# Kernel tuning notes

Hardware: AMD Instinct MI355X
Metric: run time of the kernel (lower is better)

Reference implementation:

```python
import jax, jax.numpy as jnp
import numpy as np

B, N = 32, 2048
SLOTS, PSD, VIEW = 5, 15, 9
DM, NH, MH, EGO = 64, 4, 128, 32
PAIR_D = SLOTS * (SLOTS - 1) // 2          # 10
TER_D = VIEW * VIEW                        # 81
NBR_D = SLOTS * PSD + PAIR_D               # 85
D_OBS = EGO + NBR_D + TER_D                # 198


def setup_inputs() -> dict:
    key = jax.random.key(0)
    ks = jax.random.split(key, 64)

    def _p(k, shape, s=0.05):
        return (jax.random.normal(k, shape) * s).astype(jnp.float32)

    def z(*shape):
        return jnp.zeros(shape, jnp.float32)

    # --- observation with some genuinely-masked slots (r == 0) ---
    ego = jax.random.normal(ks[0], (B, N, EGO), jnp.float32)
    nbr = jax.random.normal(ks[1], (B, N, SLOTS, PSD), jnp.float32)
    keep = jax.random.bernoulli(ks[2], 0.8, (B, N, SLOTS)).astype(jnp.float32)
    nbr = jnp.concatenate([nbr[..., 0:3] * keep[..., None], nbr[..., 3:]], axis=-1)
    pair = jax.random.normal(ks[3], (B, N, PAIR_D), jnp.float32)
    ter = jax.random.normal(ks[4], (B, N, TER_D), jnp.float32)
    obs = jnp.concatenate([ego, nbr.reshape(B, N, SLOTS * PSD), pair, ter], axis=-1)

    i = 5
    def nk():
        nonlocal i
        i += 1
        return ks[i - 1]

    params = {
        "tok_w": _p(nk(), (12, DM)), "tok_b": z(DM),
        "ln1_s": jnp.ones((DM,), jnp.float32), "ln1_b": z(DM),
        "a1_qw": _p(nk(), (DM, DM)), "a1_qb": z(DM),
        "a1_kw": _p(nk(), (DM, DM)), "a1_kb": z(DM),
        "a1_vw": _p(nk(), (DM, DM)), "a1_vb": z(DM),
        "a1_ow": _p(nk(), (DM, DM)), "a1_ob": z(DM),
        "ln2_s": jnp.ones((DM,), jnp.float32), "ln2_b": z(DM),
        "m1_w": _p(nk(), (DM, MH)), "m1_b": z(MH),
        "m2_w": _p(nk(), (MH, MH)), "m2_b": z(MH),
        "m3_w": _p(nk(), (MH, DM)), "m3_b": z(DM),
        "e1_w": _p(nk(), (EGO, MH)), "e1_b": z(MH),
        "e2_w": _p(nk(), (MH, MH)), "e2_b": z(MH),
        "e3_w": _p(nk(), (MH, DM)), "e3_b": z(DM),
        "l1_w": _p(nk(), (2 * DM, MH)), "l1_b": z(MH),
        "l2_w": _p(nk(), (MH, MH)), "l2_b": z(MH),
        "l3_w": _p(nk(), (MH, 1)), "l3_b": z(1),
        "seed": _p(nk(), (1, 1, DM), 0.02),
        "p_qw": _p(nk(), (DM, DM)), "p_qb": z(DM),
        "p_kw": _p(nk(), (DM, DM)), "p_kb": z(DM),
        "p_vw": _p(nk(), (DM, DM)), "p_vb": z(DM),
        "p_ow": _p(nk(), (DM, DM)), "p_ob": z(DM),
        "pr_w": _p(nk(), (PAIR_D, DM)), "pr_b": z(DM),
        "h1_w": _p(nk(), (EGO + 2 * DM, MH)), "h1_b": z(MH),
        "h2_w": _p(nk(), (MH, MH)), "h2_b": z(MH),
        "h3_w": _p(nk(), (MH, MH)), "h3_b": z(MH),
    }
    return {"obs": obs, **params}


def _layernorm(x, s, b, eps=1e-6):
    m = jnp.mean(x, axis=-1, keepdims=True)
    v = jnp.var(x, axis=-1, keepdims=True)
    return (x - m) * jax.lax.rsqrt(v + eps) * s + b


def _zero_if_masked(x, mask):
    return jnp.where(mask[..., None], x, jnp.array(0.0, x.dtype))


def _masked_softmax(logits, mask, eps=1e-9):
    mask = mask.astype(bool)
    very_neg = jnp.array(-1e9, logits.dtype)
    ml = jnp.where(mask, logits, very_neg)
    mx = jnp.max(ml, axis=-1, keepdims=True)
    ex = jnp.exp(ml - mx) * mask.astype(logits.dtype)
    return ex / (jnp.sum(ex, axis=-1, keepdims=True) + eps)


def _mha(q_in, kv_in, attn_mask, qw, qb, kw, kb, vw, vb, ow, ob, nh=NH):
    dm = q_in.shape[-1]
    dh = dm // nh
    q = (q_in @ qw + qb).reshape(*q_in.shape[:-1], nh, dh)
    k = (kv_in @ kw + kb).reshape(*kv_in.shape[:-1], nh, dh)
    v = (kv_in @ vw + vb).reshape(*kv_in.shape[:-1], nh, dh)
    logits = jnp.einsum('...qhd,...khd->...hqk', q, k) / jnp.sqrt(jnp.float32(dh))
    neg = jnp.finfo(logits.dtype).min
    logits = jnp.where(attn_mask, logits, neg)
    attn = jax.nn.softmax(logits, axis=-1)
    o = jnp.einsum('...hqk,...khd->...qhd', attn, v).reshape(*q_in.shape[:-1], dm)
    return o @ ow + ob


def _mlp3(x, w1, b1, w2, b2, w3, b3):
    x = jax.nn.gelu(x @ w1 + b1)
    x = jax.nn.gelu(x @ w2 + b2)
    return x @ w3 + b3


def reference(obs, tok_w, tok_b, ln1_s, ln1_b,
              a1_qw, a1_qb, a1_kw, a1_kb, a1_vw, a1_vb, a1_ow, a1_ob,
              ln2_s, ln2_b, m1_w, m1_b, m2_w, m2_b, m3_w, m3_b,
              e1_w, e1_b, e2_w, e2_b, e3_w, e3_b,
              l1_w, l1_b, l2_w, l2_b, l3_w, l3_b,
              seed, p_qw, p_qb, p_kw, p_kb, p_vw, p_vb, p_ow, p_ob,
              pr_w, pr_b, h1_w, h1_b, h2_w, h2_b, h3_w, h3_b):
    obs = obs.astype(jnp.float32)
    Bb, Nn, Dd = obs.shape
    ego = obs[..., :EGO]
    nbr_all = obs[..., EGO:EGO + NBR_D]
    nbr_main = nbr_all[..., :SLOTS * PSD].reshape(Bb, Nn, SLOTS, PSD)
    pair = nbr_all[..., SLOTS * PSD:]

    r = nbr_main[..., 0:3]
    u = nbr_main[..., 3:6]
    att = nbr_main[..., 6:9]
    fre = nbr_main[..., 9:10]
    tem = nbr_main[..., 10:11]
    inv = nbr_main[..., 11:15]

    mask = jnp.any(jnp.abs(r) > 1e-6, axis=-1)                 # (B,N,K)
    mask_any = jnp.any(mask, axis=-1, keepdims=True)           # (B,N,1)
    mask_safe = jnp.where(mask_any, mask, mask.at[..., 0].set(True))

    r_clean = jnp.nan_to_num(r, nan=0.0, posinf=0.0, neginf=0.0)
    diff = r_clean[..., :, None, :] - r_clean[..., None, :, :]
    dist = jnp.linalg.norm(diff, axis=-1)                      # (B,N,K,K)
    pair_mask = mask[..., :, None] & mask[..., None, :]
    eye = jnp.eye(SLOTS, dtype=bool)[None, None]
    valid = pair_mask & ~eye
    big = jnp.array(1e9, dist.dtype)
    dist_no_self = jnp.where(eye, big, dist)
    d_min = jnp.min(jnp.where(valid, dist_no_self, big), axis=-1, keepdims=True)
    d_sum = jnp.sum(jnp.where(valid, dist, 0.0), axis=-1, keepdims=True)
    cnt = jnp.sum(valid, axis=-1, keepdims=True).astype(dist.dtype)
    d_mean = jnp.where(cnt > 0, d_sum / (cnt + 1e-9), 0.0)
    att_norm = jnp.linalg.norm(att, axis=-1, keepdims=True)

    tok_in = jnp.concatenate([inv, fre, tem, att, att_norm, d_min, d_mean], axis=-1)  # (B,N,K,12)
    tok = jax.nn.gelu(tok_in @ tok_w + tok_b)
    tok = _zero_if_masked(tok, mask)

    # --- SetTransformerBlock ---
    qk = mask_safe[..., :, None] & mask_safe[..., None, :]
    attn_mask = qk[..., None, :, :]                            # (B,N,1,K,K)
    y = _layernorm(tok, ln1_s, ln1_b)
    y = _mha(y, y, attn_mask, a1_qw, a1_qb, a1_kw, a1_kb, a1_vw, a1_vb, a1_ow, a1_ob)
    y = _zero_if_masked(y, mask)
    tok = tok + y
    zz = _layernorm(tok, ln2_s, ln2_b)
    zz = _mlp3(zz, m1_w, m1_b, m2_w, m2_b, m3_w, m3_b)
    zz = _zero_if_masked(zz, mask)
    tok = _zero_if_masked(tok + zz, mask)

    # --- alpha weights ---
    ego_ctx = _mlp3(ego, e1_w, e1_b, e2_w, e2_b, e3_w, e3_b)   # (B,N,DM)
    ego_ctx_b = jnp.broadcast_to(ego_ctx[..., None, :], tok.shape)
    logits = _mlp3(jnp.concatenate([tok, ego_ctx_b], axis=-1),
                   l1_w, l1_b, l2_w, l2_b, l3_w, l3_b)[..., 0]
    alpha = _masked_softmax(logits, mask)
    alpha3 = alpha[..., None]
    v_r = jnp.sum(alpha3 * r, axis=-2)
    v_u = jnp.sum(alpha3 * u, axis=-2)

    # --- AttentionPool ---
    q = jnp.broadcast_to(seed, (*tok.shape[:-2], 1, DM)).astype(jnp.float32)
    pool_mask = mask_safe[..., None, None, :]                  # (B,N,1,1,K)
    c = _mha(q, tok, pool_mask, p_qw, p_qb, p_kw, p_kb, p_vw, p_vb, p_ow, p_ob)[..., 0, :]
    c = jnp.where(mask_any, c, jnp.zeros_like(c))

    pair_emb = jax.nn.gelu(pair @ pr_w + pr_b)
    h_in = jnp.concatenate([ego, c, pair_emb], axis=-1)
    h = _mlp3(h_in, h1_w, h1_b, h2_w, h2_b, h3_w, h3_b)
    return jnp.concatenate([h, v_r, v_u], axis=-1)             # (B,N,134)
```

## Files before the change

kernel.cpp:

```cpp
#include <hip/hip_runtime.h>
#include <math.h>


#define DOBS 198
#define NEG_INF_F (-3.402823466e38f)

typedef __bf16 v8bf __attribute__((ext_vector_type(8)));
typedef __bf16 v4bf __attribute__((ext_vector_type(4)));
typedef float  v4f  __attribute__((ext_vector_type(4)));

struct P {
  const float *obs,*tok_w,*tok_b,*ln1_s,*ln1_b,
    *a1_qw,*a1_qb,*a1_kw,*a1_kb,*a1_vw,*a1_vb,*a1_ow,*a1_ob,
    *ln2_s,*ln2_b,*m1_w,*m1_b,*m2_w,*m2_b,*m3_w,*m3_b,
    *e1_w,*e1_b,*e2_w,*e2_b,*e3_w,*e3_b,
    *l1_w,*l1_b,*l2_w,*l2_b,*l3_w,*l3_b,
    *seed,*p_qw,*p_qb,*p_kw,*p_kb,*p_vw,*p_vb,*p_ow,*p_ob,
    *pr_w,*pr_b,*h1_w,*h1_b,*h2_w,*h2_b,*h3_w,*h3_b;
  float* out;
};
static_assert(sizeof(P) == 51*sizeof(void*), "P layout");

#define W_A1Q 0
#define W_A1K 4096
#define W_A1V 8192
#define W_A1O 12288
#define W_M1  16384
#define W_M2  24576
#define W_M3  40960
#define W_E1  49152
#define W_E2  53248
#define W_E3  69632
#define W_L1  77824
#define W_L2  94208
#define W_PK  110592
#define W_PV  114688
#define W_PO  118784
#define W_H1  122880
#define W_H2  143360
#define W_H3  159744
#define W_END 176128
#define W_QP  176128

__global__ __launch_bounds__(256)
void prep_w(P a, __bf16* ws)
{
  if (blockIdx.x == 172){
    int t = threadIdx.x;
    if (t < 64){
      float acc = a.p_qb[t];
      for (int k=0;k<64;k++) acc += a.seed[k]*a.p_qw[k*64+t];
      ((float*)(ws + W_QP))[t] = acc;
    }
    return;
  }
  const float* srcs[18] = {a.a1_qw,a.a1_kw,a.a1_vw,a.a1_ow,a.m1_w,a.m2_w,a.m3_w,
                           a.e1_w,a.e2_w,a.e3_w,a.l1_w,a.l2_w,a.p_kw,a.p_vw,a.p_ow,
                           a.h1_w,a.h2_w,a.h3_w};
  const int Ks[18]   = {64,64,64,64,64,128,128,32,128,128,128,128,64,64,64,160,128,128};
  const int Ns[18]   = {64,64,64,64,128,128,64,128,128,64,128,128,64,64,64,128,128,128};
  const int offs[18] = {W_A1Q,W_A1K,W_A1V,W_A1O,W_M1,W_M2,W_M3,W_E1,W_E2,W_E3,
                        W_L1,W_L2,W_PK,W_PV,W_PO,W_H1,W_H2,W_H3};
  __shared__ float tile[32][33];
  int b = blockIdx.x, m = 0, acc = 0;
  for (; m < 18; m++){
    int t = (Ks[m]/32)*(Ns[m]/32);
    if (b < acc + t) break;
    acc += t;
  }
  int lt = b - acc, K = Ks[m], N = Ns[m];
  int ntile = N/32, kt = lt/ntile, nt = lt%ntile;
  int tx = threadIdx.x & 31, ty = threadIdx.x >> 5;
  const float* S = srcs[m];
  #pragma unroll
  for (int rr=0; rr<32; rr+=8)
    tile[ty+rr][tx] = S[(size_t)(kt*32+ty+rr)*N + nt*32+tx];
  __syncthreads();
  __bf16* D = ws + offs[m];
  #pragma unroll
  for (int rr=0; rr<32; rr+=8)
    D[(size_t)(nt*32+ty+rr)*K + kt*32+tx] = (__bf16)tile[tx][ty+rr];
}

__device__ __forceinline__ float gelu_f(float x){
  float t = x * fmaf(0.0356774081f, x*x, 0.7978845608f);
  float u = __builtin_amdgcn_exp2f(-2.885390082f * t);
  return x * __builtin_amdgcn_rcpf(1.0f + u);
}

__device__ __forceinline__ void load16f(const __bf16* p, float* f){
  v8bf a = *(const v8bf*)p, b = *(const v8bf*)(p+8);
  #pragma unroll
  for (int i=0;i<8;i++){ f[i]=(float)a[i]; f[8+i]=(float)b[i]; }
}

template<int KT,int MT,int NTPW,typename LA,typename E>
__device__ __forceinline__ void gemmNS(LA la, const __bf16* __restrict__ Wt,
    const float* __restrict__ bias, int wv, int lane, E epi)
{
  const int ar = lane&15, quad = lane>>4;
  #pragma unroll
  for (int ln=0; ln<NTPW; ln++){
    const int wt = wv*NTPW + ln;
    const __bf16* wp = Wt + (size_t)(wt*16+ar)*(KT*32) + quad*8;
    v8bf wf[KT];
    #pragma unroll
    for (int kt=0;kt<KT;kt++) wf[kt] = *(const v8bf*)(wp + kt*32);
    float4 b4 = *(const float4*)(bias + wt*16 + quad*4);
    #pragma unroll
    for (int mt=0; mt<MT; mt++){
      v4f c; c[0]=b4.x; c[1]=b4.y; c[2]=b4.z; c[3]=b4.w;
      #pragma unroll
      for (int kt=0;kt<KT;kt++)
        c = __builtin_amdgcn_mfma_f32_16x16x32_bf16(wf[kt], la(mt,kt,ar,quad), c, 0,0,0);
      epi(wt*16 + quad*4, mt, ar, c);
    }
  }
}

__global__ __launch_bounds__(256,3)
void swarm_mfma(P a, const __bf16* __restrict__ ws, int ntok)
{
  __shared__ char smem[53120] __attribute__((aligned(16)));
  __bf16* Ab   = (__bf16*)(smem);
  __bf16* Bb   = (__bf16*)(smem+17408);
  float*  TOKIN= (float*) (smem+17408);
  __bf16* Tk   = (__bf16*)(smem+34816);
  float*  OBSf = (float*) (smem+34816);
  __bf16* Po   = (__bf16*)(smem+34816);
  __bf16* Pe   = (__bf16*)(smem+44032);
  __bf16* Eg   = (__bf16*)(smem+46080);
  __bf16* Ru   = (__bf16*)(smem+47360);
  __bf16* mfb  = (__bf16*)(smem+48096);
  __bf16* msfb = (__bf16*)(smem+48224);
  float*  many = (float*) (smem+48352);
  float*  lga  = (float*) (smem+48416);
  __bf16* ECX  = (__bf16*)(smem+48672);
  float*  pattn= (float*) (smem+48672);
  __bf16* ATTb = (__bf16*)(smem+50720);
  __bf16* Cc   = (__bf16*)(smem+50720);

  const int lane = threadIdx.x & 63;
  const int wv   = threadIdx.x >> 6;
  const int ar   = lane & 15, quad = lane >> 4;
  const long blkT0 = (long)blockIdx.x*12;

  for (int it=lane; it<3*117; it+=64){
    int tg=it/117, c=it-tg*117;
    long gt = blkT0 + 3*wv + tg; if (gt>ntok-1) gt=ntok-1;
    OBSf[(3*wv+tg)*120+c] = a.obs[gt*DOBS+c];
  }
  float* Df = (float*)Ab;
  for (int it=lane; it<75; it+=64){
    int tg=it/25, p=it-tg*25, i=p/5, j=p-i*5;
    const float* ob = OBSf + (3*wv+tg)*120 + 32;
    float d2=0.f;
    #pragma unroll
    for (int d=0;d<3;d++){
      float ri=ob[15*i+d]; ri = isfinite(ri)?ri:0.f;
      float rj=ob[15*j+d]; rj = isfinite(rj)?rj:0.f;
      float df=ri-rj; d2 += df*df;
    }
    Df[(3*wv+tg)*32+p]=sqrtf(d2);
  }
  if (lane<15){
    int T=3*wv+lane/5, s=lane%5;
    const float* b = OBSf + T*120 + 32 + 15*s;
    mfb[15*wv+lane] = (__bf16)((fabsf(b[0])>1e-6f||fabsf(b[1])>1e-6f||fabsf(b[2])>1e-6f)?1.f:0.f);
  }
  if (wv==0 && lane>=60){ mfb[lane]=(__bf16)0.f; msfb[lane]=(__bf16)0.f; }
  if (wv==0 && lane>=12 && lane<16) many[lane]=0.f;
  if (lane<3){
    int T=3*wv+lane;
    float any = (float)mfb[T*5]+(float)mfb[T*5+1]+(float)mfb[T*5+2]+(float)mfb[T*5+3]+(float)mfb[T*5+4];
    float anyf = (any>0.f)?1.f:0.f; many[T]=anyf;
    #pragma unroll
    for (int i=0;i<5;i++) msfb[T*5+i] = (anyf>0.f)? mfb[T*5+i] : (__bf16)((i==0)?1.f:0.f);
  }
  if (lane<15){
    int T=3*wv+lane/5, i=lane%5, R=15*wv+lane;
    float dmin=1e9f,dsum=0.f,cnt=0.f;
    #pragma unroll
    for (int j=0;j<5;j++){
      if (j!=i && (float)mfb[T*5+i]>0.5f && (float)mfb[T*5+j]>0.5f){
        float dd=Df[T*32+i*5+j];
        dmin=fminf(dmin,dd); dsum+=dd; cnt+=1.f;
      }
    }
    TOKIN[R*12+10]=dmin;
    TOKIN[R*12+11]=(cnt>0.f)? dsum/(cnt+1e-9f) : 0.f;
  }
  for (int it=lane; it<150; it+=64){
    int tg=it/50, q=it-tg*50, s=q/10, c=q-s*10;
    int T=3*wv+tg;
    const float* b = OBSf + T*120 + 32 + 15*s;
    float v;
    if (c<4)        v=b[11+c];
    else if (c==4)  v=b[9];
    else if (c==5)  v=b[10];
    else if (c<9)   v=b[6+(c-6)];
    else { float a0=b[6],a1=b[7],a2=b[8]; v=sqrtf(a0*a0+a1*a1+a2*a2); }
    TOKIN[(T*5+s)*12+c]=v;
  }
  for (int it=lane; it<96; it+=64){
    int tg=it>>5, c=it&31;
    Eg[(3*wv+tg)*40+c] = (__bf16)OBSf[(3*wv+tg)*120+c];
  }
  for (int it=lane; it<90; it+=64){
    int tg=it/30, c=it-tg*30;
    Ru[(3*wv+tg)*30+c] = (__bf16)OBSf[(3*wv+tg)*120+32+15*(c/6)+(c%6)];
  }
  for (int it=lane; it<192; it+=64){
    int tg=it>>6, c=it&63;
    float acc = a.pr_b[c];
    #pragma unroll
    for (int k=0;k<10;k++) acc += OBSf[(3*wv+tg)*120+107+k]*a.pr_w[k*64+c];
    Pe[(3*wv+tg)*64+c] = (__bf16)gelu_f(acc);
  }
  __syncthreads();

  {
    float w0[12];
    #pragma unroll
    for (int k=0;k<12;k++) w0[k] = a.tok_w[k*64+lane];
    float tb = a.tok_b[lane];
    for (int r=0;r<15;r++){
      int R = 15*wv + r;
      const float4* tin = (const float4*)(TOKIN + R*12);
      float4 x0 = tin[0], x1 = tin[1], x2 = tin[2];
      float acc = tb;
      acc=fmaf(x0.x,w0[0],acc); acc=fmaf(x0.y,w0[1],acc);
      acc=fmaf(x0.z,w0[2],acc); acc=fmaf(x0.w,w0[3],acc);
      acc=fmaf(x1.x,w0[4],acc); acc=fmaf(x1.y,w0[5],acc);
      acc=fmaf(x1.z,w0[6],acc); acc=fmaf(x1.w,w0[7],acc);
      acc=fmaf(x2.x,w0[8],acc); acc=fmaf(x2.y,w0[9],acc);
      acc=fmaf(x2.z,w0[10],acc); acc=fmaf(x2.w,w0[11],acc);
      Tk[R*72+lane] = (__bf16)(gelu_f(acc)*(float)mfb[R]);
    }
  }
  if (ar<15){
    int R = 15*wv + ar;
    float x[16]; load16f(Tk + R*72 + quad*16, x);
    float s=0.f;
    #pragma unroll
    for (int i=0;i<16;i++) s += x[i];
    s += __shfl_xor(s,16,64); s += __shfl_xor(s,32,64);
    float m = s*(1.f/64.f), q=0.f;
    #pragma unroll
    for (int i=0;i<16;i++){ float d=x[i]-m; q=fmaf(d,d,q); }
    q += __shfl_xor(q,16,64); q += __shfl_xor(q,32,64);
    float rs = __builtin_amdgcn_rsqf(q*(1.f/64.f)+1e-6f);
    v8bf o0,o1;
    #pragma unroll
    for (int i=0;i<8;i++){
      o0[i]=(__bf16)((x[i]  -m)*rs*a.ln1_s[quad*16+i]  +a.ln1_b[quad*16+i]);
      o1[i]=(__bf16)((x[8+i]-m)*rs*a.ln1_s[quad*16+8+i]+a.ln1_b[quad*16+8+i]);
    }
    *(v8bf*)(Ab+R*136+quad*16)=o0; *(v8bf*)(Ab+R*136+quad*16+8)=o1;
  }
  __syncthreads();

  auto actAb = [&](int mt,int kt,int r,int q){ return *(const v8bf*)(Ab + (size_t)(mt*16+r)*136 + q*8 + kt*32); };
  auto actBb = [&](int mt,int kt,int r,int q){ return *(const v8bf*)(Bb + (size_t)(mt*16+r)*136 + q*8 + kt*32); };
  auto actTk = [&](int mt,int kt,int r,int q){ return *(const v8bf*)(Tk + (size_t)(mt*16+r)*72  + q*8 + kt*32); };

  gemmNS<2,4,1>(actAb, ws+W_A1K, a.a1_kb, wv, lane,
    [&](int wb,int mt,int r,v4f c){ v4bf o;
      #pragma unroll
      for (int k=0;k<4;k++) o[k]=(__bf16)c[k];
      *(v4bf*)&Bb[(mt*16+r)*136+64+wb]=o; });
  gemmNS<2,4,1>(actAb, ws+W_A1V, a.a1_vb, wv, lane,
    [&](int wb,int mt,int r,v4f c){ v4bf o;
      #pragma unroll
      for (int k=0;k<4;k++) o[k]=(__bf16)c[k];
      *(v4bf*)&Ab[(mt*16+r)*136+64+wb]=o; });
  gemmNS<2,4,1>(actAb, ws+W_A1Q, a.a1_qb, wv, lane,
    [&](int wb,int mt,int r,v4f c){ v4bf o;
      #pragma unroll
      for (int k=0;k<4;k++) o[k]=(__bf16)c[k];
      *(v4bf*)&Bb[(mt*16+r)*136+wb]=o; });
  __syncthreads();

  if (lane<60){
    int tg=lane/20, rem=lane-tg*20, h=rem/5, i=rem-h*5;
    int T=3*wv+tg;
    bool mi = (float)msfb[T*5+i]>0.5f;
    float qv[16]; load16f(&Bb[(T*5+i)*136 + h*16], qv);
    float lgv[5], mx=NEG_INF_F;
    #pragma unroll
    for (int j=0;j<5;j++){
      float kk[16]; load16f(&Bb[(T*5+j)*136 + 64 + h*16], kk);
      float d=0.f;
      #pragma unroll
      for (int dd=0;dd<16;dd++) d += qv[dd]*kk[dd];
      bool mj = (float)msfb[T*5+j]>0.5f;
      lgv[j] = (mi&&mj)? d*0.25f : NEG_INF_F;
      mx = fmaxf(mx,lgv[j]);
    }
    float sum=0.f, ex[5];
    #pragma unroll
    for (int j=0;j<5;j++){ ex[j]=__expf(lgv[j]-mx); sum+=ex[j]; }
    float inv=1.0f/sum;
    #pragma unroll
    for (int j=0;j<5;j++) ATTb[T*100+(h*5+i)*5+j]=(__bf16)(ex[j]*inv);
  }
  {
    int h = lane>>4;
    #pragma unroll
    for (int tg=0; tg<3; tg++){
      int T=3*wv+tg;
      float v5[5];
      #pragma unroll
      for (int j=0;j<5;j++) v5[j] = (float)Ab[(T*5+j)*136+64+lane];
      #pragma unroll
      for (int i=0;i<5;i++){
        float o=0.f;
        #pragma unroll
        for (int j=0;j<5;j++) o += (float)ATTb[T*100+(h*5+i)*5+j]*v5[j];
        Ab[(T*5+i)*136+lane]=(__bf16)o;
      }
    }
  }
  __syncthreads();

  gemmNS<2,4,1>(actAb, ws+W_A1O, a.a1_ob, wv, lane,
    [&](int wb,int mt,int r,v4f c){
      int R=mt*16+r; float mm=(float)mfb[R];
      v4bf old=*(const v4bf*)&Tk[R*72+wb]; v4bf o;
      #pragma unroll
      for (int k=0;k<4;k++) o[k]=(__bf16)((float)old[k]+c[k]*mm);
      *(v4bf*)&Tk[R*72+wb]=o; });
  __syncthreads();

  if (ar<15){
    int R = 15*wv + ar;
    float x[16]; load16f(Tk + R*72 + quad*16, x);
    float s=0.f;
    #pragma unroll
    for (int i=0;i<16;i++) s += x[i];
    s += __shfl_xor(s,16,64); s += __shfl_xor(s,32,64);
    float m = s*(1.f/64.f), q=0.f;
    #pragma unroll
    for (int i=0;i<16;i++){ float d=x[i]-m; q=fmaf(d,d,q); }
    q += __shfl_xor(q,16,64); q += __shfl_xor(q,32,64);
    float rs = __builtin_amdgcn_rsqf(q*(1.f/64.f)+1e-6f);
    v8bf o0,o1;
    #pragma unroll
    for (int i=0;i<8;i++){
      o0[i]=(__bf16)((x[i]  -m)*rs*a.ln2_s[quad*16+i]  +a.ln2_b[quad*16+i]);
      o1[i]=(__bf16)((x[8+i]-m)*rs*a.ln2_s[quad*16+8+i]+a.ln2_b[quad*16+8+i]);
    }
    *(v8bf*)(Ab+R*136+quad*16)=o0; *(v8bf*)(Ab+R*136+quad*16+8)=o1;
  }
  __syncthreads();

  gemmNS<2,4,2>(actAb, ws+W_M1, a.m1_b, wv, lane,
    [&](int wb,int mt,int r,v4f c){ v4bf o;
      #pragma unroll
      for (int k=0;k<4;k++) o[k]=(__bf16)gelu_f(c[k]);
      *(v4bf*)&Bb[(mt*16+r)*136+wb]=o; });
  __syncthreads();
  gemmNS<4,4,2>(actBb, ws+W_M2, a.m2_b, wv, lane,
    [&](int wb,int mt,int r,v4f c){ v4bf o;
      #pragma unroll
      for (int k=0;k<4;k++) o[k]=(__bf16)gelu_f(c[k]);
      *(v4bf*)&Ab[(mt*16+r)*136+wb]=o; });
  __syncthreads();
  gemmNS<4,4,1>(actAb, ws+W_M3, a.m3_b, wv, lane,
    [&](int wb,int mt,int r,v4f c){
      int R=mt*16+r; float mm=(float)mfb[R];
      v4bf old=*(const v4bf*)&Tk[R*72+wb]; v4bf o;
      #pragma unroll
      for (int k=0;k<4;k++) o[k]=(__bf16)(((float)old[k]+c[k]*mm)*mm);
      *(v4bf*)&Tk[R*72+wb]=o; });
  gemmNS<1,1,2>([&](int,int,int r,int q){ return *(const v8bf*)(Eg + (size_t)r*40 + q*8); },
    ws+W_E1, a.e1_b, wv, lane,
    [&](int wb,int mt,int r,v4f c){ v4bf o;
      #pragma unroll
      for (int k=0;k<4;k++) o[k]=(__bf16)gelu_f(c[k]);
      *(v4bf*)&Bb[r*136+wb]=o; });
  __syncthreads();
  gemmNS<4,1,2>(actBb, ws+W_E2, a.e2_b, wv, lane,
    [&](int wb,int mt,int r,v4f c){ v4bf o;
      #pragma unroll
      for (int k=0;k<4;k++) o[k]=(__bf16)gelu_f(c[k]);
      *(v4bf*)&Ab[r*136+wb]=o; });
  __syncthreads();
  gemmNS<4,1,1>(actAb, ws+W_E3, a.e3_b, wv, lane,
    [&](int wb,int mt,int r,v4f c){ v4bf o;
      #pragma unroll
      for (int k=0;k<4;k++) o[k]=(__bf16)c[k];
      *(v4bf*)&ECX[r*64+wb]=o; });
  __syncthreads();
  gemmNS<4,4,2>([&](int mt,int kt,int r,int q){
      int R=mt*16+r;
      return (kt<2) ? *(const v8bf*)(Tk + (size_t)R*72 + q*8 + kt*32)
                    : *(const v8bf*)(ECX + (size_t)((R*205)>>10)*64 + q*8 + (kt-2)*32); },
    ws+W_L1, a.l1_b, wv, lane,
    [&](int wb,int mt,int r,v4f c){ v4bf o;
      #pragma unroll
      for (int k=0;k<4;k++) o[k]=(__bf16)gelu_f(c[k]);
      *(v4bf*)&Bb[(mt*16+r)*136+wb]=o; });
  __syncthreads();
  gemmNS<4,4,2>(actBb, ws+W_L2, a.l2_b, wv, lane,
    [&](int wb,int mt,int r,v4f c){ v4bf o;
      #pragma unroll
      for (int k=0;k<4;k++) o[k]=(__bf16)gelu_f(c[k]);
      *(v4bf*)&Ab[(mt*16+r)*136+wb]=o; });
  __syncthreads();

  if (ar<15){
    int R = 15*wv + ar;
    float x[16], y[16];
    load16f(&Ab[R*136 + quad*32], x);
    load16f(&Ab[R*136 + quad*32 + 16], y);
    const float* w = a.l3_w + quad*32;
    float p = 0.f;
    #pragma unroll
    for (int i=0;i<16;i++) p = fmaf(x[i], w[i], p);
    #pragma unroll
    for (int i=0;i<16;i++) p = fmaf(y[i], w[16+i], p);
    p += __shfl_xor(p,16,64); p += __shfl_xor(p,32,64);
    if (quad==0) lga[R] = p + a.l3_b[0];
  }
  gemmNS<2,4,1>(actTk, ws+W_PK, a.p_kb, wv, lane,
    [&](int wb,int mt,int r,v4f c){ v4bf o;
      #pragma unroll
      for (int k=0;k<4;k++) o[k]=(__bf16)c[k];
      *(v4bf*)&Bb[(mt*16+r)*136+wb]=o; });
  gemmNS<2,4,1>(actTk, ws+W_PV, a.p_vb, wv, lane,
    [&](int wb,int mt,int r,v4f c){ v4bf o;
      #pragma unroll
      for (int k=0;k<4;k++) o[k]=(__bf16)c[k];
      *(v4bf*)&Bb[(mt*16+r)*136+64+wb]=o; });
  if (lane<3){
    int T=3*wv+lane;
    float ml[5], mx=-1e9f;
    #pragma unroll
    for (int i=0;i<5;i++){ ml[i]=((float)mfb[T*5+i]>0.5f)? lga[T*5+i] : -1e9f; mx=fmaxf(mx,ml[i]); }
    float den=0.f, e[5];
    #pragma unroll
    for (int i=0;i<5;i++){ e[i]=__expf(ml[i]-mx)*(float)mfb[T*5+i]; den+=e[i]; }
    float inv=1.0f/(den+1e-9f);
    #pragma unroll
    for (int i=0;i<5;i++) lga[T*5+i]=e[i]*inv;
  }
  if (lane<18){
    int tg=lane/6, c=lane-tg*6;
    int T=3*wv+tg;
    float v=0.f;
    #pragma unroll
    for (int i=0;i<5;i++) v += lga[T*5+i]*(float)Ru[T*30+i*6+c];
    long tk = blkT0 + T;
    if (tk<ntok) a.out[tk*134+128+c]=v;
  }
  __syncthreads();

  if (lane<12){
    const float* qg = (const float*)(ws + W_QP);
    int tg=lane>>2, h=lane&3;
    int T=3*wv+tg;
    float qv[16];
    #pragma unroll
    for (int dd=0;dd<16;dd++) qv[dd]=qg[h*16+dd];
    float lgv[5], mx=NEG_INF_F;
    #pragma unroll
    for (int j=0;j<5;j++){
      float kk[16]; load16f(&Bb[(T*5+j)*136 + h*16], kk);
      float d=0.f;
      #pragma unroll
      for (int dd=0;dd<16;dd++) d += qv[dd]*kk[dd];
      lgv[j] = ((float)msfb[T*5+j]>0.5f)? d*0.25f : NEG_INF_F;
      mx = fmaxf(mx,lgv[j]);
    }
    float sum=0.f, ex[5];
    #pragma unroll
    for (int j=0;j<5;j++){ ex[j]=__expf(lgv[j]-mx); sum+=ex[j]; }
    float inv=1.0f/sum;
    #pragma unroll
    for (int j=0;j<5;j++) pattn[T*20+h*5+j]=ex[j]*inv;
  }
  for (int it=lane; it<192; it+=64){
    int tg=it>>6, c=it&63, h=c>>4;
    int T=3*wv+tg;
    float o=0.f;
    #pragma unroll
    for (int j=0;j<5;j++)
      o += pattn[T*20+h*5+j]*(float)Bb[(T*5+j)*136+64+c];
    Po[T*64+c]=(__bf16)o;
  }
  __syncthreads();

  gemmNS<2,1,1>([&](int,int kt,int r,int q){ return *(const v8bf*)(Po + (size_t)r*64 + q*8 + kt*32); },
    ws+W_PO, a.p_ob, wv, lane,
    [&](int wb,int mt,int r,v4f c){
      float mm = many[r];
      v4bf o;
      #pragma unroll
      for (int k=0;k<4;k++) o[k]=(__bf16)(c[k]*mm);
      *(v4bf*)&Cc[r*64+wb]=o; });
  __syncthreads();

  gemmNS<5,1,2>([&](int,int kt,int r,int q){
      if (kt==0) return *(const v8bf*)(Eg + (size_t)r*40 + q*8);
      if (kt<3)  return *(const v8bf*)(Cc + (size_t)r*64 + q*8 + (kt-1)*32);
      return *(const v8bf*)(Pe + (size_t)r*64 + q*8 + (kt-3)*32); },
    ws+W_H1, a.h1_b, wv, lane,
    [&](int wb,int mt,int r,v4f c){ v4bf o;
      #pragma unroll
      for (int k=0;k<4;k++) o[k]=(__bf16)gelu_f(c[k]);
      *(v4bf*)&Bb[r*136+wb]=o; });
  __syncthreads();
  gemmNS<4,1,2>(actBb, ws+W_H2, a.h2_b, wv, lane,
    [&](int wb,int mt,int r,v4f c){ v4bf o;
      #pragma unroll
      for (int k=0;k<4;k++) o[k]=(__bf16)gelu_f(c[k]);
      *(v4bf*)&Ab[r*136+wb]=o; });
  __syncthreads();
  gemmNS<4,1,2>(actAb, ws+W_H3, a.h3_b, wv, lane,
    [&](int wb,int mt,int r,v4f c){
      long tk = blkT0 + r;
      if (r<12 && tk<ntok){
        float2* o2 = (float2*)&a.out[tk*134 + wb];
        o2[0] = make_float2(c[0], c[1]);
        o2[1] = make_float2(c[2], c[3]);
      } });
}

extern "C" void kernel_launch(void* const* d_in, const int* in_sizes, int n_in,
                              void* d_out, int out_size, void* d_ws, size_t ws_size,
                              hipStream_t stream)
{
  P a;
  const float** pp = reinterpret_cast<const float**>(&a);
  for (int i=0;i<50;i++) pp[i] = reinterpret_cast<const float*>(d_in[i]);
  a.out = reinterpret_cast<float*>(d_out);
  int ntok = in_sizes[0] / DOBS;

  __bf16* ws = reinterpret_cast<__bf16*>(d_ws);
  hipLaunchKernelGGL(prep_w, dim3(173), dim3(256), 0, stream, a, ws);
  hipLaunchKernelGGL(swarm_mfma, dim3((ntok+11)/12), dim3(256), 0, stream, a, ws, ntok);
}
```

Baseline: 508.5 us.

## Prefetch MFMA weight fragments into registers ahead of each GEMM stage

Splits the GEMM helper into a weight-fragment loader and a compute routine. Each layer's weight fragments are now issued as global loads one or more stages earlier, so their latency overlaps with preceding compute and barriers instead of stalling at the start of each GEMM. The cost is higher register pressure from holding several fragment sets live at once, which under launch_bounds(256,3) could cause spills or lower occupancy.

```diff
diff --git a/kernel.cpp b/kernel.cpp
--- a/kernel.cpp
+++ b/kernel.cpp
@@ -94,25 +94,37 @@
   for (int i=0;i<8;i++){ f[i]=(float)a[i]; f[8+i]=(float)b[i]; }
 }
 
+template<int KT,int NTPW> struct WF { v8bf v[NTPW*KT]; };
+
+template<int KT,int NTPW>
+__device__ __forceinline__ WF<KT,NTPW> loadW(const __bf16* __restrict__ Wt,
+                                             int wv, int lane){
+  WF<KT,NTPW> w;
+  const int ar=lane&15, quad=lane>>4;
+  #pragma unroll
+  for (int ln=0; ln<NTPW; ln++){
+    const __bf16* wp = Wt + (size_t)((wv*NTPW+ln)*16+ar)*(KT*32) + quad*8;
+    #pragma unroll
+    for (int kt=0;kt<KT;kt++) w.v[ln*KT+kt] = *(const v8bf*)(wp + kt*32);
+  }
+  return w;
+}
+
 template<int KT,int MT,int NTPW,typename LA,typename E>
-__device__ __forceinline__ void gemmNS(LA la, const __bf16* __restrict__ Wt,
-    const float* __restrict__ bias, int wv, int lane, E epi)
+__device__ __forceinline__ void gemmC(const WF<KT,NTPW>& wf,
+    const float* __restrict__ bias, int wv, int lane, LA la, E epi)
 {
-  const int ar = lane&15, quad = lane>>4;
+  const int ar=lane&15, quad=lane>>4;
   #pragma unroll
   for (int ln=0; ln<NTPW; ln++){
     const int wt = wv*NTPW + ln;
-    const __bf16* wp = Wt + (size_t)(wt*16+ar)*(KT*32) + quad*8;
-    v8bf wf[KT];
-    #pragma unroll
-    for (int kt=0;kt<KT;kt++) wf[kt] = *(const v8bf*)(wp + kt*32);
     float4 b4 = *(const float4*)(bias + wt*16 + quad*4);
     #pragma unroll
     for (int mt=0; mt<MT; mt++){
       v4f c; c[0]=b4.x; c[1]=b4.y; c[2]=b4.z; c[3]=b4.w;
       #pragma unroll
       for (int kt=0;kt<KT;kt++)
-        c = __builtin_amdgcn_mfma_f32_16x16x32_bf16(wf[kt], la(mt,kt,ar,quad), c, 0,0,0);
+        c = __builtin_amdgcn_mfma_f32_16x16x32_bf16(wf.v[ln*KT+kt], la(mt,kt,ar,quad), c, 0,0,0);
       epi(wt*16 + quad*4, mt, ar, c);
     }
   }
@@ -219,6 +231,9 @@
   }
   __syncthreads();
 
+  WF<2,1> wfK = loadW<2,1>(ws+W_A1K, wv, lane);
+  WF<2,1> wfV = loadW<2,1>(ws+W_A1V, wv, lane);
+  WF<2,1> wfQ = loadW<2,1>(ws+W_A1Q, wv, lane);
   {
     float w0[12];
     #pragma unroll
@@ -264,23 +279,25 @@
   auto actBb = [&](int mt,int kt,int r,int q){ return *(const v8bf*)(Bb + (size_t)(mt*16+r)*136 + q*8 + kt*32); };
   auto actTk = [&](int mt,int kt,int r,int q){ return *(const v8bf*)(Tk + (size_t)(mt*16+r)*72  + q*8 + kt*32); };
 
-  gemmNS<2,4,1>(actAb, ws+W_A1K, a.a1_kb, wv, lane,
+  WF<2,1> wfO = loadW<2,1>(ws+W_A1O, wv, lane);
+  gemmC<2,4,1>(wfK, a.a1_kb, wv, lane, actAb,
     [&](int wb,int mt,int r,v4f c){ v4bf o;
       #pragma unroll
       for (int k=0;k<4;k++) o[k]=(__bf16)c[k];
       *(v4bf*)&Bb[(mt*16+r)*136+64+wb]=o; });
-  gemmNS<2,4,1>(actAb, ws+W_A1V, a.a1_vb, wv, lane,
+  gemmC<2,4,1>(wfV, a.a1_vb, wv, lane, actAb,
     [&](int wb,int mt,int r,v4f c){ v4bf o;
       #pragma unroll
       for (int k=0;k<4;k++) o[k]=(__bf16)c[k];
       *(v4bf*)&Ab[(mt*16+r)*136+64+wb]=o; });
-  gemmNS<2,4,1>(actAb, ws+W_A1Q, a.a1_qb, wv, lane,
+  gemmC<2,4,1>(wfQ, a.a1_qb, wv, lane, actAb,
     [&](int wb,int mt,int r,v4f c){ v4bf o;
       #pragma unroll
       for (int k=0;k<4;k++) o[k]=(__bf16)c[k];
       *(v4bf*)&Bb[(mt*16+r)*136+wb]=o; });
   __syncthreads();
 
+  WF<2,2> wfM1 = loadW<2,2>(ws+W_M1, wv, lane);
   if (lane<60){
     int tg=lane/20, rem=lane-tg*20, h=rem/5, i=rem-h*5;
     int T=3*wv+tg;
@@ -323,7 +340,8 @@
   }
   __syncthreads();
 
-  gemmNS<2,4,1>(actAb, ws+W_A1O, a.a1_ob, wv, lane,
+  WF<4,2> wfM2 = loadW<4,2>(ws+W_M2, wv, lane);
+  gemmC<2,4,1>(wfO, a.a1_ob, wv, lane, actAb,
     [&](int wb,int mt,int r,v4f c){
       int R=mt*16+r; float mm=(float)mfb[R];
       v4bf old=*(const v4bf*)&Tk[R*72+wb]; v4bf o;
@@ -332,6 +350,8 @@
       *(v4bf*)&Tk[R*72+wb]=o; });
   __syncthreads();
 
+  WF<4,1> wfM3 = loadW<4,1>(ws+W_M3, wv, lane);
+  WF<1,2> wfE1 = loadW<1,2>(ws+W_E1, wv, lane);
   if (ar<15){
     int R = 15*wv + ar;
     float x[16]; load16f(Tk + R*72 + quad*16, x);
@@ -354,55 +374,68 @@
   }
   __syncthreads();
 
-  gemmNS<2,4,2>(actAb, ws+W_M1, a.m1_b, wv, lane,
+  WF<4,2> wfE2 = loadW<4,2>(ws+W_E2, wv, lane);
+  gemmC<2,4,2>(wfM1, a.m1_b, wv, lane, actAb,
     [&](int wb,int mt,int r,v4f c){ v4bf o;
       #pragma unroll
       for (int k=0;k<4;k++) o[k]=(__bf16)gelu_f(c[k]);
       *(v4bf*)&Bb[(mt*16+r)*136+wb]=o; });
   __syncthreads();
-  gemmNS<4,4,2>(actBb, ws+W_M2, a.m2_b, wv, lane,
+
+  WF<4,1> wfE3 = loadW<4,1>(ws+W_E3, wv, lane);
+  gemmC<4,4,2>(wfM2, a.m2_b, wv, lane, actBb,
     [&](int wb,int mt,int r,v4f c){ v4bf o;
       #pragma unroll
       for (int k=0;k<4;k++) o[k]=(__bf16)gelu_f(c[k]);
       *(v4bf*)&Ab[(mt*16+r)*136+wb]=o; });
   __syncthreads();
-  gemmNS<4,4,1>(actAb, ws+W_M3, a.m3_b, wv, lane,
+
+  WF<4,2> wfL1 = loadW<4,2>(ws+W_L1, wv, lane);
+  gemmC<4,4,1>(wfM3, a.m3_b, wv, lane, actAb,
     [&](int wb,int mt,int r,v4f c){
       int R=mt*16+r; float mm=(float)mfb[R];
       v4bf old=*(const v4bf*)&Tk[R*72+wb]; v4bf o;
       #pragma unroll
       for (int k=0;k<4;k++) o[k]=(__bf16)(((float)old[k]+c[k]*mm)*mm);
       *(v4bf*)&Tk[R*72+wb]=o; });
-  gemmNS<1,1,2>([&](int,int,int r,int q){ return *(const v8bf*)(Eg + (size_t)r*40 + q*8); },
-    ws+W_E1, a.e1_b, wv, lane,
+  gemmC<1,1,2>(wfE1, a.e1_b, wv, lane,
+    [&](int,int,int r,int q){ return *(const v8bf*)(Eg + (size_t)r*40 + q*8); },
     [&](int wb,int mt,int r,v4f c){ v4bf o;
       #pragma unroll
       for (int k=0;k<4;k++) o[k]=(__bf16)gelu_f(c[k]);
       *(v4bf*)&Bb[r*136+wb]=o; });
   __syncthreads();
-  gemmNS<4,1,2>(actBb, ws+W_E2, a.e2_b, wv, lane,
+
+  WF<4,2> wfL2 = loadW<4,2>(ws+W_L2, wv, lane);
+  gemmC<4,1,2>(wfE2, a.e2_b, wv, lane, actBb,
     [&](int wb,int mt,int r,v4f c){ v4bf o;
       #pragma unroll
       for (int k=0;k<4;k++) o[k]=(__bf16)gelu_f(c[k]);
       *(v4bf*)&Ab[r*136+wb]=o; });
   __syncthreads();
-  gemmNS<4,1,1>(actAb, ws+W_E3, a.e3_b, wv, lane,
+
+  WF<2,1> wfPK = loadW<2,1>(ws+W_PK, wv, lane);
+  WF<2,1> wfPV = loadW<2,1>(ws+W_PV, wv, lane);
+  gemmC<4,1,1>(wfE3, a.e3_b, wv, lane, actAb,
     [&](int wb,int mt,int r,v4f c){ v4bf o;
       #pragma unroll
       for (int k=0;k<4;k++) o[k]=(__bf16)c[k];
       *(v4bf*)&ECX[r*64+wb]=o; });
   __syncthreads();
-  gemmNS<4,4,2>([&](int mt,int kt,int r,int q){
+
+  gemmC<4,4,2>(wfL1, a.l1_b, wv, lane,
+    [&](int mt,int kt,int r,int q){
       int R=mt*16+r;
       return (kt<2) ? *(const v8bf*)(Tk + (size_t)R*72 + q*8 + kt*32)
                     : *(const v8bf*)(ECX + (size_t)((R*205)>>10)*64 + q*8 + (kt-2)*32); },
-    ws+W_L1, a.l1_b, wv, lane,
     [&](int wb,int mt,int r,v4f c){ v4bf o;
       #pragma unroll
       for (int k=0;k<4;k++) o[k]=(__bf16)gelu_f(c[k]);
       *(v4bf*)&Bb[(mt*16+r)*136+wb]=o; });
   __syncthreads();
-  gemmNS<4,4,2>(actBb, ws+W_L2, a.l2_b, wv, lane,
+
+  WF<2,1> wfPO = loadW<2,1>(ws+W_PO, wv, lane);
+  gemmC<4,4,2>(wfL2, a.l2_b, wv, lane, actBb,
     [&](int wb,int mt,int r,v4f c){ v4bf o;
       #pragma unroll
       for (int k=0;k<4;k++) o[k]=(__bf16)gelu_f(c[k]);
@@ -423,12 +456,12 @@
     p += __shfl_xor(p,16,64); p += __shfl_xor(p,32,64);
     if (quad==0) lga[R] = p + a.l3_b[0];
   }
-  gemmNS<2,4,1>(actTk, ws+W_PK, a.p_kb, wv, lane,
+  gemmC<2,4,1>(wfPK, a.p_kb, wv, lane, actTk,
     [&](int wb,int mt,int r,v4f c){ v4bf o;
       #pragma unroll
       for (int k=0;k<4;k++) o[k]=(__bf16)c[k];
       *(v4bf*)&Bb[(mt*16+r)*136+wb]=o; });
-  gemmNS<2,4,1>(actTk, ws+W_PV, a.p_vb, wv, lane,
+  gemmC<2,4,1>(wfPV, a.p_vb, wv, lane, actTk,
     [&](int wb,int mt,int r,v4f c){ v4bf o;
       #pragma unroll
       for (int k=0;k<4;k++) o[k]=(__bf16)c[k];
@@ -456,6 +489,7 @@
   }
   __syncthreads();
 
+  WF<5,2> wfH1 = loadW<5,2>(ws+W_H1, wv, lane);
   if (lane<12){
     const float* qg = (const float*)(ws + W_QP);
     int tg=lane>>2, h=lane&3;
@@ -491,8 +525,9 @@
   }
   __syncthreads();
 
-  gemmNS<2,1,1>([&](int,int kt,int r,int q){ return *(const v8bf*)(Po + (size_t)r*64 + q*8 + kt*32); },
-    ws+W_PO, a.p_ob, wv, lane,
+  WF<4,2> wfH2 = loadW<4,2>(ws+W_H2, wv, lane);
+  gemmC<2,1,1>(wfPO, a.p_ob, wv, lane,
+    [&](int,int kt,int r,int q){ return *(const v8bf*)(Po + (size_t)r*64 + q*8 + kt*32); },
     [&](int wb,int mt,int r,v4f c){
       float mm = many[r];
       v4bf o;
@@ -501,23 +536,26 @@
       *(v4bf*)&Cc[r*64+wb]=o; });
   __syncthreads();
 
-  gemmNS<5,1,2>([&](int,int kt,int r,int q){
+  WF<4,2> wfH3 = loadW<4,2>(ws+W_H3, wv, lane);
+  gemmC<5,1,2>(wfH1, a.h1_b, wv, lane,
+    [&](int,int kt,int r,int q){
       if (kt==0) return *(const v8bf*)(Eg + (size_t)r*40 + q*8);
       if (kt<3)  return *(const v8bf*)(Cc + (size_t)r*64 + q*8 + (kt-1)*32);
       return *(const v8bf*)(Pe + (size_t)r*64 + q*8 + (kt-3)*32); },
-    ws+W_H1, a.h1_b, wv, lane,
     [&](int wb,int mt,int r,v4f c){ v4bf o;
       #pragma unroll
       for (int k=0;k<4;k++) o[k]=(__bf16)gelu_f(c[k]);
       *(v4bf*)&Bb[r*136+wb]=o; });
   __syncthreads();
-  gemmNS<4,1,2>(actBb, ws+W_H2, a.h2_b, wv, lane,
+
+  gemmC<4,1,2>(wfH2, a.h2_b, wv, lane, actBb,
     [&](int wb,int mt,int r,v4f c){ v4bf o;
       #pragma unroll
       for (int k=0;k<4;k++) o[k]=(__bf16)gelu_f(c[k]);
       *(v4bf*)&Ab[r*136+wb]=o; });
   __syncthreads();
-  gemmNS<4,1,2>(actAb, ws+W_H3, a.h3_b, wv, lane,
+
+  gemmC<4,1,2>(wfH3, a.h3_b, wv, lane, actAb,
     [&](int wb,int mt,int r,v4f c){
       long tk = blkT0 + r;
       if (r<12 && tk<ntok){
```

New measurement: 524.0 us. +3.0%, slower.
